# Optimization experiments

Hardware: AMD Instinct MI355X
Metric: run time of the kernel (lower is better)

## Reference

```python
import jax, jax.numpy as jnp
import numpy as np

E = 8        # num_experts
D = 512      # embed_size
H = 8        # attention heads
HD = D // H  # head dim
B, S = 4, 1024


def setup_inputs() -> dict:
    key = jax.random.key(0)
    ks = jax.random.split(key, 16)
    sd = 0.02
    return {
        "x":  jax.random.normal(ks[0], (B, S, D), jnp.float32),
        # per-expert FFN params, stacked over expert dim
        "W1": jax.random.normal(ks[1], (E, D, 4 * D), jnp.float32) * sd,
        "b1": jnp.zeros((E, 4 * D), jnp.float32),
        "W2": jax.random.normal(ks[2], (E, 4 * D, D), jnp.float32) * sd,
        "b2": jnp.zeros((E, D), jnp.float32),
        # MultiheadAttention in_proj (split) and out_proj
        "Wq": jax.random.normal(ks[3], (D, D), jnp.float32) * sd,
        "bq": jnp.zeros((D,), jnp.float32),
        "Wk": jax.random.normal(ks[4], (D, D), jnp.float32) * sd,
        "bk": jnp.zeros((D,), jnp.float32),
        "Wv": jax.random.normal(ks[5], (D, D), jnp.float32) * sd,
        "bv": jnp.zeros((D,), jnp.float32),
        "Wo": jax.random.normal(ks[6], (D, D), jnp.float32) * sd,
        "bo": jnp.zeros((D,), jnp.float32),
        "expert_id": 3,
    }


def reference(x, W1, b1, W2, b2, Wq, bq, Wk, bk, Wv, bv, Wo, bo, expert_id):
    # --- batched per-expert FFN (fuses the Python loop over experts) ---
    # hidden: [B, E, S, 4D]
    hidden = jax.nn.relu(jnp.einsum('bsd,edf->besf', x, W1) + b1[None, :, None, :])
    eo = jnp.einsum('besf,efd->besd', hidden, W2) + b2[None, :, None, :]  # [B,E,S,D]
    eo = eo.transpose(0, 2, 1, 3)  # [B, S, E, D]

    Bs, Ss = x.shape[0], x.shape[1]
    a = eo.reshape(Bs * Ss, E, D)  # [N, E, D]; attention runs over the expert dim

    # --- MultiheadAttention (batch_first), torch semantics ---
    # NOTE: the original passes a FLOAT tril-of-ones attn_mask, which torch ADDS
    # to the scores (it does NOT mask with -inf). We reproduce that faithfully.
    q = (a @ Wq.T + bq).reshape(-1, E, H, HD).transpose(0, 2, 1, 3)  # [N,H,E,hd]
    k = (a @ Wk.T + bk).reshape(-1, E, H, HD).transpose(0, 2, 1, 3)
    v = (a @ Wv.T + bv).reshape(-1, E, H, HD).transpose(0, 2, 1, 3)

    mask = jnp.tril(jnp.ones((E, E), jnp.float32))  # additive float mask
    scores = jnp.einsum('nhed,nhfd->nhef', q, k) / jnp.sqrt(jnp.float32(HD))
    scores = scores + mask[None, None, :, :]
    attn = jax.nn.softmax(scores, axis=-1)
    ctx = jnp.einsum('nhef,nhfd->nhed', attn, v)           # [N,H,E,hd]
    ctx = ctx.transpose(0, 2, 1, 3).reshape(-1, E, D)       # [N,E,D]
    out = ctx @ Wo.T + bo                                   # [N,E,D]

    out = out.reshape(Bs, Ss, E, D)
    return out[:, :, expert_id, :]  # [B, S, D]
```

## Files before the change

### kernel.cpp

```cpp
#include <hip/hip_runtime.h>
#include <hip/hip_bf16.h>

typedef __hip_bfloat16 bf16;
typedef __attribute__((ext_vector_type(4))) float f32x4;
typedef __attribute__((ext_vector_type(8))) short s16x8;

#define N_TOK 4096
#define Dm    512
#define Fm    2048
#define Em    8

__device__ __forceinline__ float bf2f(bf16 v) { return __bfloat162float(v); }
__device__ __forceinline__ bf16  f2bf(float f) { return __float2bfloat16(f); }

#define GL16(g, l)                                                              \
  __builtin_amdgcn_global_load_lds(                                             \
      (const __attribute__((address_space(1))) void*)(g),                       \
      (__attribute__((address_space(3))) void*)(l), 16, 0, 0)

#define BAR()                                   \
  do {                                          \
    __builtin_amdgcn_s_barrier();               \
    asm volatile("" ::: "memory");              \
  } while (0)

__global__ void cvt_f32_bf16(const float* __restrict__ in, bf16* __restrict__ out, int n4) {
  int i = blockIdx.x * 256 + threadIdx.x;
  if (i >= n4) return;
  float4 v = reinterpret_cast<const float4*>(in)[i];
  bf16 tmp[4] = {f2bf(v.x), f2bf(v.y), f2bf(v.z), f2bf(v.w)};
  __builtin_memcpy(out + (size_t)i * 4, tmp, 8);
}

__global__ void cvt_weights(const float* __restrict__ Wq, const float* __restrict__ Wk,
                            const float* __restrict__ Wv, const float* __restrict__ Wo,
                            const float* __restrict__ bk, const float* __restrict__ bv,
                            bf16* __restrict__ qw, bf16* __restrict__ kvw,
                            bf16* __restrict__ ow, float* __restrict__ bkv) {
  int b = blockIdx.x;
  if (b < 1024) {
    int which = b >> 8;
    int i = (b & 255) * 256 + threadIdx.x;
    const float* src = which == 0 ? Wq : which == 1 ? Wk : which == 2 ? Wv : Wo;
    bf16* dst = which == 0 ? qw : which == 1 ? kvw
              : which == 2 ? (kvw + (size_t)Dm * Dm) : ow;
    float4 v = reinterpret_cast<const float4*>(src)[i];
    bf16 tmp[4] = {f2bf(v.x), f2bf(v.y), f2bf(v.z), f2bf(v.w)};
    __builtin_memcpy(dst + (size_t)i * 4, tmp, 8);
  } else {
    for (int j = threadIdx.x; j < Dm; j += 256) {
      bkv[j] = bk[j];
      bkv[Dm + j] = bv[j];
    }
  }
}

__global__ void transpose_cvt(const float* __restrict__ in, bf16* __restrict__ out,
                              int R, int C, long inb, long outb) {
  in  += (long)blockIdx.z * inb;
  out += (long)blockIdx.z * outb;
  __shared__ float t[32][33];
  int tx = threadIdx.x & 31, ty = threadIdx.x >> 5;
  int c0 = blockIdx.x * 32, r0 = blockIdx.y * 32;
#pragma unroll
  for (int i = 0; i < 32; i += 8)
    t[ty + i][tx] = in[(long)(r0 + ty + i) * C + c0 + tx];
  __syncthreads();
#pragma unroll
  for (int i = 0; i < 32; i += 8)
    out[(long)(c0 + ty + i) * R + r0 + tx] = f2bf(t[tx][ty + i]);
}

template <bool RELU, bool OUT_BF16>
__global__ __launch_bounds__(256, 4) void gemm128d(
    const bf16* __restrict__ A, const bf16* __restrict__ Bt, void* __restrict__ Cout,
    const float* __restrict__ bias, int K, int lda, int ldb, int ldc,
    long abs_, long bbs, long cbs, long biasbs,
    const int* __restrict__ eid, int eid_scale) {
  __shared__ bf16 As[2][128 * 32];
  __shared__ bf16 Bs[2][128 * 32];

  int e = blockIdx.z;
  A    += (long)e * abs_;
  Bt   += (long)e * bbs;
  bias += (long)e * biasbs;
  long coff = (long)e * cbs;
  if (eid) A += (long)(*eid) * eid_scale;

  int bm = blockIdx.x * 128, bn = blockIdx.y * 128;
  int tid = threadIdx.x, wv = tid >> 6, lane = tid & 63;
  int wm = wv >> 1, wn = wv & 1;
  int la = lane & 15, q = lane >> 4;
  int srow = lane >> 2;

  const bf16* Ab = A + (long)bm * lda;
  const bf16* Bb = Bt + (long)bn * ldb;
  int nt = K >> 5;

  auto stage = [&](int t) {
    if (t >= nt) return;
    int k0 = t << 5;
    bf16* abuf = &As[t & 1][0];
    bf16* bbuf = &Bs[t & 1][0];
#pragma unroll
    for (int i = 0; i < 2; ++i) {
      int r = wv * 32 + i * 16 + srow;
      int c = (lane & 3) ^ ((r >> 1) & 3);
      GL16(Ab + (long)r * lda + k0 + c * 8, abuf + (wv * 32 + i * 16) * 32);
      GL16(Bb + (long)r * ldb + k0 + c * 8, bbuf + (wv * 32 + i * 16) * 32);
    }
  };

  f32x4 acc[4][4] = {};

  stage(0);

  for (int t = 0; t < nt; ++t) {
    asm volatile("s_waitcnt vmcnt(0)" ::: "memory");
    BAR();
    stage(t + 1);
    const bf16* Abuf = &As[t & 1][0];
    const bf16* Bbuf = &Bs[t & 1][0];
    s16x8 af[4], bfr[4];
#pragma unroll
    for (int m = 0; m < 4; ++m) {
      int r = wm * 64 + m * 16 + la;
      af[m] = *reinterpret_cast<const s16x8*>(Abuf + r * 32 + (q ^ ((r >> 1) & 3)) * 8);
    }
#pragma unroll
    for (int n = 0; n < 4; ++n) {
      int r = wn * 64 + n * 16 + la;
      bfr[n] = *reinterpret_cast<const s16x8*>(Bbuf + r * 32 + (q ^ ((r >> 1) & 3)) * 8);
    }
    __builtin_amdgcn_s_setprio(1);
#pragma unroll
    for (int m = 0; m < 4; ++m)
#pragma unroll
      for (int n = 0; n < 4; ++n)
        acc[m][n] = __builtin_amdgcn_mfma_f32_16x16x32_bf16(bfr[n], af[m], acc[m][n], 0, 0, 0);
    __builtin_amdgcn_s_setprio(0);
  }

#pragma unroll
  for (int m = 0; m < 4; ++m) {
    int gm = bm + wm * 64 + m * 16 + la;
#pragma unroll
    for (int n = 0; n < 4; ++n) {
      int gn = bn + wn * 64 + n * 16 + q * 4;
      float4 b4 = *reinterpret_cast<const float4*>(bias + gn);
      float v0 = acc[m][n][0] + b4.x, v1 = acc[m][n][1] + b4.y;
      float v2 = acc[m][n][2] + b4.z, v3 = acc[m][n][3] + b4.w;
      if (RELU) {
        v0 = fmaxf(v0, 0.f); v1 = fmaxf(v1, 0.f);
        v2 = fmaxf(v2, 0.f); v3 = fmaxf(v3, 0.f);
      }
      long idx = coff + (long)gm * ldc + gn;
      if (OUT_BF16) {
        bf16 tmp[4] = {f2bf(v0), f2bf(v1), f2bf(v2), f2bf(v3)};
        __builtin_memcpy((bf16*)Cout + idx, tmp, 8);
      } else {
        float tmp[4] = {v0, v1, v2, v3};
        __builtin_memcpy((float*)Cout + idx, tmp, 16);
      }
    }
  }
}

__global__ __launch_bounds__(256) void attn_kernel(const float* __restrict__ q,
                                                   const bf16* __restrict__ kv,
                                                   bf16* __restrict__ ctx,
                                                   const int* __restrict__ eid) {
  int wave = threadIdx.x >> 6, lane = threadIdx.x & 63;
  int n = blockIdx.x * 4 + wave;
  int h = lane >> 3, f = lane & 7;
  int e3 = *eid;
  const bf16* kvn = kv + (long)n * Em * (2 * Dm);
  const float* qh = q + (long)n * Dm + h * 64;
  const bf16* kf = kvn + f * (2 * Dm) + h * 64;
  float s = 0.f;
#pragma unroll
  for (int j = 0; j < 64; j++) s += qh[j] * bf2f(kf[j]);
  s *= 0.125f;
  s += (f <= e3) ? 1.0f : 0.0f;
  float mx = s;
#pragma unroll
  for (int d = 1; d < 8; d <<= 1) mx = fmaxf(mx, __shfl_xor(mx, d));
  float ex = expf(s - mx);
  float sm = ex;
#pragma unroll
  for (int d = 1; d < 8; d <<= 1) sm += __shfl_xor(sm, d);
  float at = ex / sm;
  int g = f;
  float acc[8] = {0, 0, 0, 0, 0, 0, 0, 0};
#pragma unroll
  for (int f2 = 0; f2 < 8; f2++) {
    float a = __shfl(at, (h << 3) | f2);
    const bf16* vf = kvn + f2 * (2 * Dm) + Dm + h * 64 + g * 8;
#pragma unroll
    for (int j = 0; j < 8; j++) acc[j] += a * bf2f(vf[j]);
  }
  bf16 tmp[8];
#pragma unroll
  for (int j = 0; j < 8; j++) tmp[j] = f2bf(acc[j]);
  __builtin_memcpy(ctx + (long)n * Dm + h * 64 + g * 8, tmp, 16);
}

extern "C" void kernel_launch(void* const* d_in, const int* in_sizes, int n_in,
                              void* d_out, int out_size, void* d_ws, size_t ws_size,
                              hipStream_t stream) {
  const float* x  = (const float*)d_in[0];
  const float* W1 = (const float*)d_in[1];
  const float* b1 = (const float*)d_in[2];
  const float* W2 = (const float*)d_in[3];
  const float* b2 = (const float*)d_in[4];
  const float* Wq = (const float*)d_in[5];
  const float* bq = (const float*)d_in[6];
  const float* Wk = (const float*)d_in[7];
  const float* bk = (const float*)d_in[8];
  const float* Wv = (const float*)d_in[9];
  const float* bv = (const float*)d_in[10];
  const float* Wo = (const float*)d_in[11];
  const float* bo = (const float*)d_in[12];
  const int* eid  = (const int*)d_in[13];

  char* w = (char*)d_ws;
  auto alloc = [&](size_t bytes) {
    char* p = w;
    w += (bytes + 255) & ~(size_t)255;
    return p;
  };
  bf16* xb   = (bf16*)alloc((size_t)N_TOK * Dm * 2);
  bf16* W1t  = (bf16*)alloc((size_t)Em * Fm * Dm * 2);
  bf16* W2t  = (bf16*)alloc((size_t)Em * Dm * Fm * 2);
  bf16* qw   = (bf16*)alloc((size_t)Dm * Dm * 2);
  bf16* kvw  = (bf16*)alloc((size_t)2 * Dm * Dm * 2);
  bf16* ow   = (bf16*)alloc((size_t)Dm * Dm * 2);
  float* bkv = (float*)alloc((size_t)2 * Dm * 4);
  bf16* hid  = (bf16*)alloc((size_t)Em * N_TOK * Fm * 2);
  bf16* eo   = (bf16*)alloc((size_t)N_TOK * Em * Dm * 2);
  bf16* kv   = (bf16*)hid;
  float* qb  = (float*)(hid + (size_t)N_TOK * Em * 2 * Dm);
  bf16* ctxb = (bf16*)(qb + (size_t)N_TOK * Dm);

  cvt_f32_bf16<<<(N_TOK * Dm / 4 + 255) / 256, 256, 0, stream>>>(x, xb, N_TOK * Dm / 4);
  transpose_cvt<<<dim3(Fm / 32, Dm / 32, Em), 256, 0, stream>>>(
      W1, W1t, Dm, Fm, (long)Dm * Fm, (long)Fm * Dm);
  transpose_cvt<<<dim3(Dm / 32, Fm / 32, Em), 256, 0, stream>>>(
      W2, W2t, Fm, Dm, (long)Fm * Dm, (long)Dm * Fm);
  cvt_weights<<<1025, 256, 0, stream>>>(Wq, Wk, Wv, Wo, bk, bv, qw, kvw, ow, bkv);

  gemm128d<true, true><<<dim3(32, 16, Em), 256, 0, stream>>>(
      xb, W1t, hid, b1, Dm, Dm, Dm, Fm,
      0L, (long)Fm * Dm, (long)N_TOK * Fm, (long)Fm, nullptr, 0);
  gemm128d<false, true><<<dim3(32, 4, Em), 256, 0, stream>>>(
      hid, W2t, eo, b2, Fm, Fm, Fm, Em * Dm,
      (long)N_TOK * Fm, (long)Dm * Fm, (long)Dm, (long)Dm, nullptr, 0);
  gemm128d<false, true><<<dim3(256, 8, 1), 256, 0, stream>>>(
      eo, kvw, kv, bkv, Dm, Dm, Dm, 2 * Dm,
      0L, 0L, 0L, 0L, nullptr, 0);
  gemm128d<false, false><<<dim3(32, 4, 1), 256, 0, stream>>>(
      eo, qw, qb, bq, Dm, Em * Dm, Dm, Dm,
      0L, 0L, 0L, 0L, eid, Dm);
  attn_kernel<<<N_TOK / 4, 256, 0, stream>>>(qb, kv, ctxb, eid);
  gemm128d<false, false><<<dim3(32, 4, 1), 256, 0, stream>>>(
      ctxb, ow, (float*)d_out, bo, Dm, Dm, Dm, Dm,
      0L, 0L, 0L, 0L, nullptr, 0);
}
```

Measured before the change: 327.8 us.

## Overlap next-tile loads with compute in GEMM and merge conversion kernels

The GEMM main loop now issues the next stage's LDS loads before waiting, and waits only for the current stage with a partial vmcnt, adding a second barrier per iteration. This lets global loads overlap the MFMA work. The x and attention-weight conversions are merged into one launch, removing a kernel launch. The transpose-convert kernel now writes four bf16 values per thread in one vector store instead of scattered scalar stores.

Measured after the change: 329.3 us. About the same (+0.5%).

```diff
diff --git a/kernel.cpp b/kernel.cpp
--- a/kernel.cpp
+++ b/kernel.cpp
@@ -18,29 +18,28 @@
       (const __attribute__((address_space(1))) void*)(g),                       \
       (__attribute__((address_space(3))) void*)(l), 16, 0, 0)
 
-#define BAR()                                   \
+#define RBAR()                                  \
   do {                                          \
     __builtin_amdgcn_s_barrier();               \
     asm volatile("" ::: "memory");              \
   } while (0)
 
-__global__ void cvt_f32_bf16(const float* __restrict__ in, bf16* __restrict__ out, int n4) {
-  int i = blockIdx.x * 256 + threadIdx.x;
-  if (i >= n4) return;
-  float4 v = reinterpret_cast<const float4*>(in)[i];
-  bf16 tmp[4] = {f2bf(v.x), f2bf(v.y), f2bf(v.z), f2bf(v.w)};
-  __builtin_memcpy(out + (size_t)i * 4, tmp, 8);
-}
-
-__global__ void cvt_weights(const float* __restrict__ Wq, const float* __restrict__ Wk,
-                            const float* __restrict__ Wv, const float* __restrict__ Wo,
-                            const float* __restrict__ bk, const float* __restrict__ bv,
-                            bf16* __restrict__ qw, bf16* __restrict__ kvw,
-                            bf16* __restrict__ ow, float* __restrict__ bkv) {
+__global__ void cvt_all(const float* __restrict__ x, const float* __restrict__ Wq,
+                        const float* __restrict__ Wk, const float* __restrict__ Wv,
+                        const float* __restrict__ Wo, const float* __restrict__ bk,
+                        const float* __restrict__ bv, bf16* __restrict__ xb,
+                        bf16* __restrict__ qw, bf16* __restrict__ kvw,
+                        bf16* __restrict__ ow, float* __restrict__ bkv) {
   int b = blockIdx.x;
-  if (b < 1024) {
-    int which = b >> 8;
-    int i = (b & 255) * 256 + threadIdx.x;
+  if (b < 2048) {
+    int i = b * 256 + threadIdx.x;
+    float4 v = reinterpret_cast<const float4*>(x)[i];
+    bf16 tmp[4] = {f2bf(v.x), f2bf(v.y), f2bf(v.z), f2bf(v.w)};
+    __builtin_memcpy(xb + (size_t)i * 4, tmp, 8);
+  } else if (b < 3072) {
+    int bb = b - 2048;
+    int which = bb >> 8;
+    int i = (bb & 255) * 256 + threadIdx.x;
     const float* src = which == 0 ? Wq : which == 1 ? Wk : which == 2 ? Wv : Wo;
     bf16* dst = which == 0 ? qw : which == 1 ? kvw
               : which == 2 ? (kvw + (size_t)Dm * Dm) : ow;
@@ -60,19 +59,22 @@
   in  += (long)blockIdx.z * inb;
   out += (long)blockIdx.z * outb;
   __shared__ float t[32][33];
-  int tx = threadIdx.x & 31, ty = threadIdx.x >> 5;
+  int tid = threadIdx.x;
+  int col = tid & 31, row8 = tid >> 5;
   int c0 = blockIdx.x * 32, r0 = blockIdx.y * 32;
 #pragma unroll
-  for (int i = 0; i < 32; i += 8)
-    t[ty + i][tx] = in[(long)(r0 + ty + i) * C + c0 + tx];
+  for (int i = 0; i < 4; ++i)
+    t[row8 + i * 8][col] = in[(long)(r0 + row8 + i * 8) * C + c0 + col];
   __syncthreads();
-#pragma unroll
-  for (int i = 0; i < 32; i += 8)
-    out[(long)(c0 + ty + i) * R + r0 + tx] = f2bf(t[tx][ty + i]);
+  int cc = tid >> 3, rb = (tid & 7) * 4;
+  bf16 tmp[4];
+#pragma unroll
+  for (int k = 0; k < 4; ++k) tmp[k] = f2bf(t[rb + k][cc]);
+  __builtin_memcpy(out + (long)(c0 + cc) * R + r0 + rb, tmp, 8);
 }
 
 template <bool RELU, bool OUT_BF16>
-__global__ __launch_bounds__(256, 4) void gemm128d(
+__global__ __launch_bounds__(256, 4) void gemm128p(
     const bf16* __restrict__ A, const bf16* __restrict__ Bt, void* __restrict__ Cout,
     const float* __restrict__ bias, int K, int lda, int ldb, int ldc,
     long abs_, long bbs, long cbs, long biasbs,
@@ -80,14 +82,15 @@
   __shared__ bf16 As[2][128 * 32];
   __shared__ bf16 Bs[2][128 * 32];
 
-  int e = blockIdx.z;
+  int e  = blockIdx.z;
+  int bm = blockIdx.x * 128, bn = blockIdx.y * 128;
+
   A    += (long)e * abs_;
   Bt   += (long)e * bbs;
   bias += (long)e * biasbs;
   long coff = (long)e * cbs;
   if (eid) A += (long)(*eid) * eid_scale;
 
-  int bm = blockIdx.x * 128, bn = blockIdx.y * 128;
   int tid = threadIdx.x, wv = tid >> 6, lane = tid & 63;
   int wm = wv >> 1, wn = wv & 1;
   int la = lane & 15, q = lane >> 4;
@@ -116,9 +119,12 @@
   stage(0);
 
   for (int t = 0; t < nt; ++t) {
-    asm volatile("s_waitcnt vmcnt(0)" ::: "memory");
-    BAR();
+    RBAR();
     stage(t + 1);
+    if (t + 1 < nt) asm volatile("s_waitcnt vmcnt(4)" ::: "memory");
+    else            asm volatile("s_waitcnt vmcnt(0)" ::: "memory");
+    RBAR();
+
     const bf16* Abuf = &As[t & 1][0];
     const bf16* Bbuf = &Bs[t & 1][0];
     s16x8 af[4], bfr[4];
@@ -242,27 +248,26 @@
   float* qb  = (float*)(hid + (size_t)N_TOK * Em * 2 * Dm);
   bf16* ctxb = (bf16*)(qb + (size_t)N_TOK * Dm);
 
-  cvt_f32_bf16<<<(N_TOK * Dm / 4 + 255) / 256, 256, 0, stream>>>(x, xb, N_TOK * Dm / 4);
+  cvt_all<<<3073, 256, 0, stream>>>(x, Wq, Wk, Wv, Wo, bk, bv, xb, qw, kvw, ow, bkv);
   transpose_cvt<<<dim3(Fm / 32, Dm / 32, Em), 256, 0, stream>>>(
       W1, W1t, Dm, Fm, (long)Dm * Fm, (long)Fm * Dm);
   transpose_cvt<<<dim3(Dm / 32, Fm / 32, Em), 256, 0, stream>>>(
       W2, W2t, Fm, Dm, (long)Fm * Dm, (long)Dm * Fm);
-  cvt_weights<<<1025, 256, 0, stream>>>(Wq, Wk, Wv, Wo, bk, bv, qw, kvw, ow, bkv);
-
-  gemm128d<true, true><<<dim3(32, 16, Em), 256, 0, stream>>>(
+
+  gemm128p<true, true><<<dim3(32, 16, Em), 256, 0, stream>>>(
       xb, W1t, hid, b1, Dm, Dm, Dm, Fm,
       0L, (long)Fm * Dm, (long)N_TOK * Fm, (long)Fm, nullptr, 0);
-  gemm128d<false, true><<<dim3(32, 4, Em), 256, 0, stream>>>(
+  gemm128p<false, true><<<dim3(32, 4, Em), 256, 0, stream>>>(
       hid, W2t, eo, b2, Fm, Fm, Fm, Em * Dm,
       (long)N_TOK * Fm, (long)Dm * Fm, (long)Dm, (long)Dm, nullptr, 0);
-  gemm128d<false, true><<<dim3(256, 8, 1), 256, 0, stream>>>(
+  gemm128p<false, true><<<dim3(256, 8, 1), 256, 0, stream>>>(
       eo, kvw, kv, bkv, Dm, Dm, Dm, 2 * Dm,
       0L, 0L, 0L, 0L, nullptr, 0);
-  gemm128d<false, false><<<dim3(32, 4, 1), 256, 0, stream>>>(
+  gemm128p<false, false><<<dim3(32, 4, 1), 256, 0, stream>>>(
       eo, qw, qb, bq, Dm, Em * Dm, Dm, Dm,
       0L, 0L, 0L, 0L, eid, Dm);
   attn_kernel<<<N_TOK / 4, 256, 0, stream>>>(qb, kv, ctxb, eid);
-  gemm128d<false, false><<<dim3(32, 4, 1), 256, 0, stream>>>(
+  gemm128p<false, false><<<dim3(32, 4, 1), 256, 0, stream>>>(
       ctxb, ow, (float*)d_out, bo, Dm, Dm, Dm, Dm,
       0L, 0L, 0L, 0L, nullptr, 0);
 }
```
